# Kernel optimization log

Hardware: AMD Instinct MI355X
Metric: run time of the kernel (lower is better)

Reference implementation:

```python
import jax, jax.numpy as jnp
import numpy as np
import math

# config constants (match init_kwargs)
N_HEAD = 16
KNN_NUM = 4
MEM_FRAC = 4.0
BOOKKEEPING_FRAC = 0.0
RESID_ONLY = False
RESID_FOUND = 0.5   # set_resid_frac(resid_frac): found/current mix
RESID_CURR = 0.5
KNN_INFLUENCE = 1.0
NEG_INF = jnp.finfo(jnp.float32).min


def setup_inputs() -> dict:
    key = jax.random.key(0)
    k1, k2, k3, k4, k5 = jax.random.split(key, 5)
    B, T, C = 1, 2048, 1024
    H, d = N_HEAD, C // N_HEAD
    M = 8192  # per-head memory-store entries
    return {
        "x": jax.random.normal(k1, (B, T, C), jnp.float32),
        "c_attn_w": jax.random.normal(k2, (3 * C, C), jnp.float32) * 0.02,
        "c_proj_w": jax.random.normal(k3, (C, C), jnp.float32) * 0.02,
        "key_store": jax.random.normal(k4, (H, M, d), jnp.float32),
        "value_store": jax.random.normal(k5, (H, M, d), jnp.float32),
    }


def _knn_get(att, k, q, v, key_store, value_store):
    # att: (B,H,T,T), k/q/v: (B,H,T,d), stores: (H,M,d). B must be 1 (original
    # scatter offset i*t is only consistent for b==1).
    B, H, T, d = k.shape
    scale = 1.0 / math.sqrt(d)
    att_last = att[:, :, -1, :]                     # (B,H,T) last-query column
    # bookkeeping_frac == 0.0 -> skipped; mem_frac truthy -> threshold filter
    mask = att_last >= (1.0 / (MEM_FRAC * T))       # nonzero after zeroing

    # per-head flattened token lists, shape (H, N=B*T, d)
    kh = jnp.swapaxes(k, 0, 1).reshape(H, B * T, d)
    qh = jnp.swapaxes(q, 0, 1).reshape(H, B * T, d)
    vh = jnp.swapaxes(v, 0, 1).reshape(H, B * T, d)
    mask_h = jnp.swapaxes(mask, 0, 1).reshape(H, B * T)

    # exact L2 kNN (FAISS IndexFlatL2 equivalent): d2[h,n,m] = ||kh - ks||^2
    d2 = (jnp.sum(kh * kh, -1)[:, :, None]
          - 2.0 * jnp.einsum('hnd,hmd->hnm', kh, key_store)
          + jnp.sum(key_store * key_store, -1)[:, None, :])
    _, idx = jax.lax.top_k(-d2, KNN_NUM)            # (H,N,K) nearest indices

    h_ix = jnp.arange(H)[:, None, None]
    keys_found = key_store[h_ix, idx]               # (H,N,K,d)
    vals_found = value_store[h_ix, idx]
    keys_found = jnp.moveaxis(keys_found, 2, 0)     # (K,H,N,d)
    vals_found = jnp.moveaxis(vals_found, 2, 0)
    if not RESID_ONLY:
        keys_found = jnp.concatenate([kh[None], keys_found], axis=0)  # (K+1,H,N,d)
        vals_found = jnp.concatenate([vh[None], vals_found], axis=0)

    attf = jnp.einsum('khnd,hnd->khn', keys_found, qh) * scale
    attf = jnp.where(jnp.isnan(attf), NEG_INF, attf)
    attf = jax.nn.softmax(attf * KNN_INFLUENCE, axis=0)
    vals_new = jnp.einsum('khn,khnd->hnd', attf, vals_found)
    if RESID_FOUND > 0 or RESID_CURR > 0:
        vals_new = vals_new * RESID_FOUND + vh * RESID_CURR

    v_out = jnp.where(mask_h[..., None], vals_new, vh)   # scatter-equivalent
    return jnp.swapaxes(v_out.reshape(H, B, T, d), 0, 1)  # (B,H,T,d)


def reference(x, c_attn_w, c_proj_w, key_store, value_store):
    B, T, C = x.shape
    H, d = N_HEAD, C // N_HEAD
    qkv = x @ c_attn_w.T                             # (B,T,3C)
    q, k, v = jnp.split(qkv, 3, axis=2)
    q = jnp.swapaxes(q.reshape(B, T, H, d), 1, 2)    # (B,H,T,d)
    k = jnp.swapaxes(k.reshape(B, T, H, d), 1, 2)
    v = jnp.swapaxes(v.reshape(B, T, H, d), 1, 2)

    att = jnp.einsum('bhqd,bhkd->bhqk', q, k) * (1.0 / math.sqrt(d))
    causal = jnp.tril(jnp.ones((T, T), bool))
    att = jnp.where(causal, att, NEG_INF)
    att = jax.nn.softmax(att, axis=-1)

    # knn_get is @torch.no_grad() in the original -> stop_gradient
    v_new = jax.lax.stop_gradient(
        _knn_get(att, k, q, v, key_store, value_store))

    y = jnp.einsum('bhqk,bhkd->bhqd', att, v_new)
    y = jnp.swapaxes(y, 1, 2).reshape(B, T, C)
    return y @ c_proj_w.T
```

## Files before the change

kernel.cpp:

```cpp
#include <hip/hip_runtime.h>
#include <hip/hip_bf16.h>
#include <math.h>

#define TT 2048
#define CC 1024
#define HH 16
#define DDIM 64
#define MM 8192
#define C3 3072
#define SBIAS 256.0f

typedef __bf16 bf16x8 __attribute__((ext_vector_type(8)));
typedef float f32x4 __attribute__((ext_vector_type(4)));

__device__ __forceinline__ float waveReduceSum(float v) {
#pragma unroll
  for (int off = 32; off > 0; off >>= 1) v += __shfl_xor(v, off, 64);
  return v;
}
__device__ __forceinline__ unsigned umn(unsigned a, unsigned b){ return a<b?a:b; }
__device__ __forceinline__ unsigned umx(unsigned a, unsigned b){ return a>b?a:b; }
__device__ __forceinline__ unsigned umed3(unsigned a, unsigned b, unsigned c){
  unsigned d;
  asm("v_med3_u32 %0, %1, %2, %3" : "=v"(d) : "v"(a), "v"(b), "v"(c));
  return d;
}

__device__ __forceinline__ void gload16(const void* g, void* l) {
  __builtin_amdgcn_global_load_lds(
      (const __attribute__((address_space(1))) unsigned int*)g,
      (__attribute__((address_space(3))) unsigned int*)l, 16, 0, 0);
}

__global__ __launch_bounds__(256) void conv_split_k(const float* __restrict__ src,
    __hip_bfloat16* __restrict__ hi, __hip_bfloat16* __restrict__ lo)
{
  size_t i = (size_t)blockIdx.x*256 + threadIdx.x;
  const float4* p = (const float4*)(src + i*8);
  float4 a = p[0], b = p[1];
  float v[8] = {a.x,a.y,a.z,a.w,b.x,b.y,b.z,b.w};
  bf16x8 H, L;
#pragma unroll
  for (int e = 0; e < 8; ++e) {
    __bf16 hb = (__bf16)v[e];
    H[e] = hb;
    L[e] = (__bf16)(v[e] - (float)hb);
  }
  *reinterpret_cast<bf16x8*>(hi + i*8) = H;
  *reinterpret_cast<bf16x8*>(lo + i*8) = L;
}

__global__ __launch_bounds__(256) void conv_bf16_k(const float* __restrict__ src,
    __hip_bfloat16* __restrict__ dst)
{
  size_t i = (size_t)blockIdx.x*256 + threadIdx.x;
  const float4* p = (const float4*)(src + i*8);
  float4 a = p[0], b = p[1];
  float v[8] = {a.x,a.y,a.z,a.w,b.x,b.y,b.z,b.w};
  bf16x8 H;
#pragma unroll
  for (int e = 0; e < 8; ++e) H[e] = (__bf16)v[e];
  *reinterpret_cast<bf16x8*>(dst + i*8) = H;
}

__global__ __launch_bounds__(256) void conv_ks_k(const float* __restrict__ ks,
    __hip_bfloat16* __restrict__ ksb, float* __restrict__ ksn, unsigned* __restrict__ knhl)
{
  int row = blockIdx.x*4 + (threadIdx.x>>6);
  int lane = threadIdx.x & 63;
  float v = ks[(size_t)row*64 + lane];
  float sq = waveReduceSum(v*v);
  ksb[(size_t)row*64 + lane] = __float2bfloat16(-2.f*v);
  if (lane == 0) {
    ksn[row] = sq;
    float b = sq + SBIAS;
    __hip_bfloat16 hb = __float2bfloat16(b);
    float hf = __bfloat162float(hb);
    __hip_bfloat16 lb = __float2bfloat16(b - hf);
    unsigned h16 = (unsigned)__builtin_bit_cast(unsigned short, hb);
    unsigned l16 = (unsigned)__builtin_bit_cast(unsigned short, lb);
    knhl[row] = (l16 << 16) | h16;
  }
}

__global__ __launch_bounds__(256) void conv_kb_k(const float* __restrict__ qkv,
    __hip_bfloat16* __restrict__ kb)
{
  int e = blockIdx.x*256 + threadIdx.x;
  int dg = e & 7; int t = (e>>3) & (TT-1); int h = e >> 14;
  const float* src = qkv + (size_t)t*C3 + CC + h*64 + dg*8;
  __hip_bfloat16* dst = kb + ((size_t)(h*TT + t)*64 + dg*8);
#pragma unroll
  for (int i = 0; i < 8; ++i) dst[i] = __float2bfloat16(src[i]);
}

__global__ __launch_bounds__(256) void vtrans_k(const float* __restrict__ vnew,
    __hip_bfloat16* __restrict__ vbT)
{
  __shared__ float tbuf[64][65];
  const int h = blockIdx.y, t0 = blockIdx.x*64, tid = threadIdx.x;
#pragma unroll
  for (int r = 0; r < 16; ++r) {
    int e = r*256 + tid; int row = e>>6, dv = e&63;
    tbuf[row][dv] = vnew[((size_t)h*TT + t0 + row)*64 + dv];
  }
  __syncthreads();
#pragma unroll
  for (int r = 0; r < 16; ++r) {
    int e = r*256 + tid; int dv = e>>6, tt = e&63;
    vbT[((size_t)h*64 + dv)*TT + t0 + tt] = __float2bfloat16(tbuf[tt][dv]);
  }
}

template<bool SPLIT>
__global__ __launch_bounds__(256) void gemm_mfma_k(
    const __hip_bfloat16* __restrict__ Ah, const __hip_bfloat16* __restrict__ Al,
    const __hip_bfloat16* __restrict__ Bh, const __hip_bfloat16* __restrict__ Bl,
    float* __restrict__ Cc, int M, int N, int K)
{
  __shared__ __align__(16) char lds[2][32768];
  const int tid = threadIdx.x;
  const int nbx = N >> 7;
  const int by = blockIdx.x / nbx, bx = blockIdx.x - by*nbx;
  const int m0 = by << 7, n0 = bx << 7;
  const int w = tid >> 6;
  const int l = tid & 63;
  const int wslot = w << 6;
  const int wi = w >> 1, wj = w & 1;
  const int fr = l & 15, fo = l >> 4;
  const int kw = SPLIT ? 32 : 64;
  const int nsteps = K / kw;

  f32x4 acc[4][4];
#pragma unroll
  for (int i = 0; i < 4; ++i)
#pragma unroll
    for (int j = 0; j < 4; ++j) acc[i][j] = f32x4{0.f,0.f,0.f,0.f};

  int srow[4], schg[4];
#pragma unroll
  for (int r = 0; r < 4; ++r) {
    int s = r*256 + tid;
    srow[r] = s >> 3;
    schg[r] = (s & 7) ^ (srow[r] & 7);
  }

  auto stageAB = [&](int buf, int st) {
    const int k0 = st * kw;
#pragma unroll
    for (int r = 0; r < 4; ++r) {
      const __hip_bfloat16 *pa, *pb;
      if (SPLIT) {
        pa = (schg[r] < 4 ? Ah : Al) + (size_t)(m0+srow[r])*K + k0 + (schg[r]&3)*8;
        pb = (schg[r] < 4 ? Bh : Bl) + (size_t)(n0+srow[r])*K + k0 + (schg[r]&3)*8;
      } else {
        pa = Ah + (size_t)(m0+srow[r])*K + k0 + schg[r]*8;
        pb = Bh + (size_t)(n0+srow[r])*K + k0 + schg[r]*8;
      }
      gload16(pa, lds[buf] + (r*256 + wslot)*16);
      gload16(pb, lds[buf] + 16384 + (r*256 + wslot)*16);
    }
  };

  stageAB(0, 0);
  __syncthreads();

  for (int st = 0; st < nsteps; ++st) {
    const int buf = st & 1;
    if (st + 1 < nsteps) stageAB(buf ^ 1, st + 1);
    char* ldsb = lds[buf];

    if (SPLIT) {
      bf16x8 bhf[4], blf[4];
#pragma unroll
      for (int j = 0; j < 4; ++j) {
        int row = wj*64 + j*16 + fr;
        bhf[j] = *(const bf16x8*)(ldsb + 16384 + row*128 + ((fo     ^ (row&7))*16));
        blf[j] = *(const bf16x8*)(ldsb + 16384 + row*128 + (((4+fo) ^ (row&7))*16));
      }
#pragma unroll
      for (int i = 0; i < 4; ++i) {
        int row = wi*64 + i*16 + fr;
        bf16x8 ah = *(const bf16x8*)(ldsb + row*128 + ((fo     ^ (row&7))*16));
        bf16x8 al = *(const bf16x8*)(ldsb + row*128 + (((4+fo) ^ (row&7))*16));
#pragma unroll
        for (int j = 0; j < 4; ++j) {
          acc[i][j] = __builtin_amdgcn_mfma_f32_16x16x32_bf16(al, bhf[j], acc[i][j], 0,0,0);
          acc[i][j] = __builtin_amdgcn_mfma_f32_16x16x32_bf16(ah, blf[j], acc[i][j], 0,0,0);
          acc[i][j] = __builtin_amdgcn_mfma_f32_16x16x32_bf16(ah, bhf[j], acc[i][j], 0,0,0);
        }
      }
    } else {
#pragma unroll
      for (int kk = 0; kk < 2; ++kk) {
        bf16x8 bf[4];
#pragma unroll
        for (int j = 0; j < 4; ++j) {
          int row = wj*64 + j*16 + fr;
          bf[j] = *(const bf16x8*)(ldsb + 16384 + row*128 + (((kk*4+fo) ^ (row&7))*16));
        }
#pragma unroll
        for (int i = 0; i < 4; ++i) {
          int row = wi*64 + i*16 + fr;
          bf16x8 af = *(const bf16x8*)(ldsb + row*128 + (((kk*4+fo) ^ (row&7))*16));
#pragma unroll
          for (int j = 0; j < 4; ++j)
            acc[i][j] = __builtin_amdgcn_mfma_f32_16x16x32_bf16(af, bf[j], acc[i][j], 0,0,0);
        }
      }
    }
    __syncthreads();
  }

  float* ep = (float*)((char*)lds + (size_t)w*8704);
#pragma unroll
  for (int pass = 0; pass < 2; ++pass) {
#pragma unroll
    for (int ii = 0; ii < 2; ++ii) {
      int i = pass*2 + ii;
#pragma unroll
      for (int j = 0; j < 4; ++j)
#pragma unroll
        for (int e = 0; e < 4; ++e)
          ep[(ii*16 + fo*4 + e)*68 + j*16 + fr] = acc[i][j][e];
    }
#pragma unroll
    for (int eidx = 0; eidx < 8; ++eidx) {
      int fi = eidx*64 + l;
      int row = fi >> 4, c4 = fi & 15;
      float4 v4 = *(const float4*)(ep + row*68 + c4*4);
      *(float4*)(Cc + (size_t)(m0 + wi*64 + pass*32 + row)*N + n0 + wj*64 + c4*4) = v4;
    }
  }
}

__global__ __launch_bounds__(256) void attlast_mask_k(const float* __restrict__ qkv, int* __restrict__ mask)
{
  const int h = blockIdx.x;
  __shared__ float ql[64];
  __shared__ float lg[TT];
  __shared__ float red[256];
  const int tid = threadIdx.x;
  if (tid < 64) ql[tid] = qkv[(size_t)(TT-1)*C3 + h*DDIM + tid];
  __syncthreads();
  float lmax = -INFINITY;
  for (int t = tid; t < TT; t += 256) {
    const float* kr = qkv + (size_t)t*C3 + CC + h*DDIM;
    float s = 0.f;
#pragma unroll
    for (int d = 0; d < 64; ++d) s += ql[d] * kr[d];
    s *= 0.125f;
    lg[t] = s;
    lmax = fmaxf(lmax, s);
  }
  red[tid] = lmax; __syncthreads();
  for (int off = 128; off > 0; off >>= 1) { if (tid < off) red[tid] = fmaxf(red[tid], red[tid+off]); __syncthreads(); }
  float mx = red[0];
  __syncthreads();
  float ls = 0.f;
  for (int t = tid; t < TT; t += 256) { float e = expf(lg[t]-mx); lg[t] = e; ls += e; }
  red[tid] = ls; __syncthreads();
  for (int off = 128; off > 0; off >>= 1) { if (tid < off) red[tid] += red[tid+off]; __syncthreads(); }
  float Z = red[0];
  for (int t = tid; t < TT; t += 256) mask[h*TT + t] = (lg[t]/Z >= 1.220703125e-4f) ? 1 : 0;
}

__global__ __launch_bounds__(256) void knn_chunkmin_k(
    const __hip_bfloat16* __restrict__ kb, const __hip_bfloat16* __restrict__ ksb,
    const unsigned* __restrict__ knhl, unsigned int* __restrict__ cand)
{
  __shared__ __align__(16) char lds[2*8192];
  const int tid = threadIdx.x;
  const int bid = blockIdx.x;
  const int orig = (bid & 7)*64 + (bid >> 3);
  const int h  = orig >> 5;
  const int n0 = (orig & 31) * 64;
  const int w  = tid >> 6;
  const int l  = tid & 63;
  const int cr = l & 15, hi = l >> 4;

  bf16x8 af0, af1;
  {
    const __hip_bfloat16* kbh = kb + (size_t)h*TT*64 + (size_t)(n0 + w*16 + cr)*64;
    af0 = *reinterpret_cast<const bf16x8*>(kbh + hi*8);
    af1 = *reinterpret_cast<const bf16x8*>(kbh + 32 + hi*8);
  }
  bf16x8 aext;
  {
    uint4 t = { (l < 16) ? 0x3F803F80u : 0u, 0u, 0u, 0u };
    aext = __builtin_bit_cast(bf16x8, t);
  }
  const __hip_bfloat16* ksbh = ksb + (size_t)h*MM*64;
  const unsigned* knh = knhl + (size_t)h*MM;

  const int s0 = tid, s1 = tid + 256;
  const int g0 = (s0 & ~7) | ((s0 & 7) ^ ((s0 >> 3) & 7));
  const int g1 = (s1 & ~7) | ((s1 & 7) ^ ((s1 >> 3) & 7));
  const int rb0 = (l&15)*128 + ((hi ^ (l&7))*16);
  const int rb1 = (l&15)*128 + (((4+hi) ^ (l&7))*16);

  unsigned cnd[4][4];
#pragma unroll
  for (int i = 0; i < 4; ++i)
#pragma unroll
    for (int c = 0; c < 4; ++c) cnd[i][c] = 0xFFFFFFFFu;

  auto stage = [&](int buf, int tt) {
    const __hip_bfloat16* src = ksbh + (size_t)tt*4096;
    gload16(src + g0*8, lds + buf*8192 + (w << 10));
    gload16(src + g1*8, lds + buf*8192 + 4096 + (w << 10));
  };

  stage(0, 0);
  __syncthreads();

  for (int tt = 0; tt < 128; ++tt) {
    const int buf = tt & 1;
    if (tt + 1 < 128) stage(buf ^ 1, tt + 1);
    char* ldsb = lds + buf*8192;
    const unsigned crtt = ((unsigned)cr << 7) | (unsigned)tt;

    f32x4 acc[4];
#pragma unroll
    for (int b = 0; b < 4; ++b) {
      uint4 kt = { knh[tt*64 + b*16 + cr], 0u, 0u, 0u };
      bf16x8 bext = __builtin_bit_cast(bf16x8, kt);
      bf16x8 bf0 = *reinterpret_cast<const bf16x8*>(ldsb + b*2048 + rb0);
      bf16x8 bf1 = *reinterpret_cast<const bf16x8*>(ldsb + b*2048 + rb1);
      f32x4 z = {0.f, 0.f, 0.f, 0.f};
      z = __builtin_amdgcn_mfma_f32_16x16x32_bf16(aext, bext, z, 0, 0, 0);
      z = __builtin_amdgcn_mfma_f32_16x16x32_bf16(af0, bf0, z, 0, 0, 0);
      z = __builtin_amdgcn_mfma_f32_16x16x32_bf16(af1, bf1, z, 0, 0, 0);
      acc[b] = z;
    }
#pragma unroll
    for (int i = 0; i < 4; ++i) {
      float m4 = fminf(fminf(fminf(acc[0][i], acc[1][i]), acc[2][i]), acc[3][i]);
      unsigned x = (__float_as_uint(m4) & 0xFFFFF800u) | crtt;
      unsigned t0 = umn(cnd[i][0], x);
      unsigned t1 = umed3(x, cnd[i][0], cnd[i][1]);
      unsigned t2 = umed3(x, cnd[i][1], cnd[i][2]);
      unsigned t3 = umed3(x, cnd[i][2], cnd[i][3]);
      cnd[i][0] = t0; cnd[i][1] = t1; cnd[i][2] = t2; cnd[i][3] = t3;
    }
    __syncthreads();
  }

#pragma unroll
  for (int i = 0; i < 4; ++i) {
    int n = n0 + w*16 + hi*4 + i;
    reinterpret_cast<uint4*>(cand)[(size_t)(h*TT + n)*16 + cr] =
        make_uint4(cnd[i][0], cnd[i][1], cnd[i][2], cnd[i][3]);
  }
}

__global__ __launch_bounds__(256) void knn_fused_k(
    const unsigned int* __restrict__ cand, const float* __restrict__ qkv,
    const float* __restrict__ kstore, const float* __restrict__ vstore,
    const float* __restrict__ ksn, const int* __restrict__ mask,
    float* __restrict__ vnew)
{
  const int row = blockIdx.x*4 + (threadIdx.x>>6);
  const int l = threadIdx.x & 63;
  const int h = row >> 11, t = row & (TT-1);
  const float* base = qkv + (size_t)t*C3 + h*64;
  float vh = base[2*CC + l];
  float* outp = vnew + (size_t)row*64;
  if (!mask[row]) { outp[l] = vh; return; }

  unsigned v = cand[(size_t)row*64 + l];
#pragma unroll
  for (int k = 2; k <= 64; k <<= 1)
#pragma unroll
    for (int j = k>>1; j > 0; j >>= 1) {
      unsigned o = __shfl_xor(v, j, 64);
      bool takeMin = ((l & j) == 0) == ((l & k) == 0);
      v = (takeMin == (o < v)) ? o : v;
    }

  const int c = l >> 1;
  const int b = c & 3;
  unsigned vc = __shfl(v, c >> 2, 64);
  const int m = ((int)(vc & 127u))*64 + b*16 + (int)((vc >> 7) & 15u);
  const int p = l & 1;
  {
    const float* kq = base + CC + p*32;
    const float* ksr = kstore + ((size_t)h*MM + m)*64 + p*32;
    float dp = 0.f;
#pragma unroll
    for (int i = 0; i < 8; ++i) {
      float4 a = *(const float4*)(kq + i*4);
      float4 bb = *(const float4*)(ksr + i*4);
      dp = fmaf(a.x,bb.x, fmaf(a.y,bb.y, fmaf(a.z,bb.z, fmaf(a.w,bb.w, dp))));
    }
    dp += __shfl_xor(dp, 1, 64);
    float s = ksn[(size_t)h*MM + m] - 2.f*dp;
    unsigned u = __float_as_uint(s);
    unsigned skey = u ^ (unsigned)(((int)u >> 31) | 0x80000000);
    unsigned khi = (p == 0) ? skey : 0xFFFFFFFFu;
    unsigned klo = (p == 0) ? (unsigned)m : 0xFFFFFFFFu;
#pragma unroll
    for (int k = 2; k <= 64; k <<= 1)
#pragma unroll
      for (int j = k>>1; j > 0; j >>= 1) {
        unsigned oh = __shfl_xor(khi, j, 64);
        unsigned ol = __shfl_xor(klo, j, 64);
        bool takeMin = ((l & j) == 0) == ((l & k) == 0);
        bool oLess = (oh < khi) || (oh == khi && ol < klo);
        if (takeMin == oLess) { khi = oh; klo = ol; }
      }
    v = klo;
  }

  const int m0 = (int)__shfl(v, 0, 64);
  const int m1 = (int)__shfl(v, 1, 64);
  const int m2 = (int)__shfl(v, 2, 64);
  const int m3 = (int)__shfl(v, 3, 64);
  const int g = l >> 3, gl = l & 7;
  float dq = 0.f;
  if (g < 5) {
    int msel = (g == 0) ? m0 : (g == 1) ? m1 : (g == 2) ? m2 : m3;
    const float* qrow = base + gl*8;
    const float* kr = (g < 4) ? (kstore + ((size_t)h*MM + msel)*64 + gl*8)
                              : (base + CC + gl*8);
    float4 a0 = *(const float4*)(qrow);
    float4 a1 = *(const float4*)(qrow + 4);
    float4 b0 = *(const float4*)(kr);
    float4 b1 = *(const float4*)(kr + 4);
    dq = a0.x*b0.x + a0.y*b0.y + a0.z*b0.z + a0.w*b0.w
       + a1.x*b1.x + a1.y*b1.y + a1.z*b1.z + a1.w*b1.w;
  }
  dq += __shfl_xor(dq, 1, 64);
  dq += __shfl_xor(dq, 2, 64);
  dq += __shfl_xor(dq, 4, 64);
  float d0 = __shfl(dq,  0, 64)*0.125f;
  float d1 = __shfl(dq,  8, 64)*0.125f;
  float d2 = __shfl(dq, 16, 64)*0.125f;
  float d3 = __shfl(dq, 24, 64)*0.125f;
  float d4 = __shfl(dq, 32, 64)*0.125f;
  float mx = fmaxf(fmaxf(fmaxf(d0,d1),fmaxf(d2,d3)),d4);
  float w0 = expf(d0-mx), w1 = expf(d1-mx), w2 = expf(d2-mx),
        w3 = expf(d3-mx), w4 = expf(d4-mx);
  float Z = w0+w1+w2+w3+w4;
  float vv = w4*vh
           + w0*vstore[((size_t)h*MM+m0)*64 + l]
           + w1*vstore[((size_t)h*MM+m1)*64 + l]
           + w2*vstore[((size_t)h*MM+m2)*64 + l]
           + w3*vstore[((size_t)h*MM+m3)*64 + l];
  outp[l] = 0.5f*(vv/Z) + 0.5f*vh;
}

__global__ __launch_bounds__(256) void attn_mfma_k(
    const float* __restrict__ qkv, const __hip_bfloat16* __restrict__ kb,
    const __hip_bfloat16* __restrict__ vbT, __hip_bfloat16* __restrict__ yb)
{
  __shared__ __align__(16) char lds[40960];
  const int h = blockIdx.y, bx = blockIdx.x, tid = threadIdx.x;
  const int w = tid>>6, l = tid&63, fr = l&15, fo = l>>4;
  const int wslot = w << 6;
  const __hip_bfloat16* kbh = kb + (size_t)h*TT*64;
  const __hip_bfloat16* vbh = vbT + (size_t)h*64*TT;
  char* Pt = lds + 32768 + w*2048;

  int srow[2], schg[2];
#pragma unroll
  for (int r = 0; r < 2; ++r) {
    int s = r*256 + tid;
    srow[r] = s >> 3;
    schg[r] = (s & 7) ^ (srow[r] & 7);
  }

  auto stageKV = [&](int buf, int kt) {
#pragma unroll
    for (int r = 0; r < 2; ++r) {
      gload16(kbh + (size_t)(kt*64 + srow[r])*64 + schg[r]*8,
              lds + buf*16384 + (r*256 + wslot)*16);
      gload16(vbh + (size_t)srow[r]*TT + kt*64 + schg[r]*8,
              lds + buf*16384 + 8192 + (r*256 + wslot)*16);
    }
  };

  for (int half = 0; half < 2; ++half) {
    const int qblk = half ? (31 - bx) : bx;
    const int q0 = qblk * 64;
    bf16x8 qa[2];
    {
      const float* qrow = qkv + (size_t)(q0 + w*16 + fr)*C3 + h*64;
#pragma unroll
      for (int kk = 0; kk < 2; ++kk) {
        float4 u0 = *(const float4*)(qrow + kk*32 + fo*8);
        float4 u1 = *(const float4*)(qrow + kk*32 + fo*8 + 4);
        bf16x8 t;
        t[0]=(__bf16)u0.x; t[1]=(__bf16)u0.y; t[2]=(__bf16)u0.z; t[3]=(__bf16)u0.w;
        t[4]=(__bf16)u1.x; t[5]=(__bf16)u1.y; t[6]=(__bf16)u1.z; t[7]=(__bf16)u1.w;
        qa[kk] = t;
      }
    }
    float mrow[4], lsum[4];
    f32x4 oacc[4];
#pragma unroll
    for (int e = 0; e < 4; ++e) { mrow[e] = -INFINITY; lsum[e] = 0.f; }
#pragma unroll
    for (int jv = 0; jv < 4; ++jv) oacc[jv] = f32x4{0.f,0.f,0.f,0.f};

    const int ntiles = qblk + 1;
    stageKV(0, 0);
    __syncthreads();

    for (int kt = 0; kt < ntiles; ++kt) {
      const int buf = kt & 1;
      if (kt + 1 < ntiles) stageKV(buf ^ 1, kt + 1);
      char* Kt = lds + buf*16384;
      char* Vt = Kt + 8192;

      f32x4 sv[4];
#pragma unroll
      for (int j = 0; j < 4; ++j) {
        int row = j*16 + fr;
        bf16x8 k0f = *(const bf16x8*)(Kt + row*128 + ((fo     ^ (row&7))*16));
        bf16x8 k1f = *(const bf16x8*)(Kt + row*128 + (((4+fo) ^ (row&7))*16));
        f32x4 z = {0.f,0.f,0.f,0.f};
        z = __builtin_amdgcn_mfma_f32_16x16x32_bf16(qa[0], k0f, z, 0,0,0);
        z = __builtin_amdgcn_mfma_f32_16x16x32_bf16(qa[1], k1f, z, 0,0,0);
        sv[j] = z;
      }
      if (kt == qblk) {
#pragma unroll
        for (int j = 0; j < 4; ++j)
#pragma unroll
          for (int e = 0; e < 4; ++e)
            sv[j][e] = (j*16 + fr <= w*16 + fo*4 + e) ? sv[j][e]*0.125f : -INFINITY;
      } else {
#pragma unroll
        for (int j = 0; j < 4; ++j)
#pragma unroll
          for (int e = 0; e < 4; ++e) sv[j][e] *= 0.125f;
      }
      float rmax[4];
#pragma unroll
      for (int e = 0; e < 4; ++e)
        rmax[e] = fmaxf(fmaxf(sv[0][e], sv[1][e]), fmaxf(sv[2][e], sv[3][e]));
#pragma unroll
      for (int off = 1; off < 16; off <<= 1)
#pragma unroll
        for (int e = 0; e < 4; ++e) rmax[e] = fmaxf(rmax[e], __shfl_xor(rmax[e], off, 64));
      float scl[4];
#pragma unroll
      for (int e = 0; e < 4; ++e) {
        float mn = fmaxf(mrow[e], rmax[e]);
        scl[e] = __expf(mrow[e] - mn);
        mrow[e] = mn;
      }
      float rsum[4] = {0.f,0.f,0.f,0.f};
#pragma unroll
      for (int j = 0; j < 4; ++j) {
        int chunkbase = j*2 + (fr>>3);
        int kvoff = (fr&7)*2;
#pragma unroll
        for (int e = 0; e < 4; ++e) {
          float p = __expf(sv[j][e] - mrow[e]);
          rsum[e] += p;
          int qloc = fo*4 + e;
          *(__bf16*)(Pt + qloc*128 + ((chunkbase ^ (qloc&7))*16) + kvoff) = (__bf16)p;
        }
      }
#pragma unroll
      for (int off = 1; off < 16; off <<= 1)
#pragma unroll
        for (int e = 0; e < 4; ++e) rsum[e] += __shfl_xor(rsum[e], off, 64);
#pragma unroll
      for (int e = 0; e < 4; ++e) lsum[e] = lsum[e]*scl[e] + rsum[e];
#pragma unroll
      for (int jv = 0; jv < 4; ++jv)
#pragma unroll
        for (int e = 0; e < 4; ++e) oacc[jv][e] *= scl[e];

      bf16x8 pa0 = *(const bf16x8*)(Pt + fr*128 + ((fo     ^ (fr&7))*16));
      bf16x8 pa1 = *(const bf16x8*)(Pt + fr*128 + (((4+fo) ^ (fr&7))*16));
#pragma unroll
      for (int jv = 0; jv < 4; ++jv) {
        int row = jv*16 + fr;
        bf16x8 v0f = *(const bf16x8*)(Vt + row*128 + ((fo     ^ (row&7))*16));
        bf16x8 v1f = *(const bf16x8*)(Vt + row*128 + (((4+fo) ^ (row&7))*16));
        oacc[jv] = __builtin_amdgcn_mfma_f32_16x16x32_bf16(pa0, v0f, oacc[jv], 0,0,0);
        oacc[jv] = __builtin_amdgcn_mfma_f32_16x16x32_bf16(pa1, v1f, oacc[jv], 0,0,0);
      }
      __syncthreads();
    }
#pragma unroll
    for (int jv = 0; jv < 4; ++jv)
#pragma unroll
      for (int e = 0; e < 4; ++e) {
        int t = q0 + w*16 + fo*4 + e;
        yb[(size_t)t*CC + h*64 + jv*16 + fr] = __float2bfloat16(oacc[jv][e] / lsum[e]);
      }
  }
}

extern "C" void kernel_launch(void* const* d_in, const int* in_sizes, int n_in,
                              void* d_out, int out_size, void* d_ws, size_t ws_size,
                              hipStream_t stream) {
  const float* x   = (const float*)d_in[0];
  const float* wat = (const float*)d_in[1];
  const float* wpr = (const float*)d_in[2];
  const float* kst = (const float*)d_in[3];
  const float* vst = (const float*)d_in[4];
  float* out = (float*)d_out;

  float* ws    = (float*)d_ws;
  float* qkv   = ws;
  float* ksn   = qkv + (size_t)6291456;
  unsigned* knhl = (unsigned*)(ksn + 131072);
  int*   idxb  = (int*)(knhl + 131072);
  int*   maskb = idxb + 131072;
  __hip_bfloat16* kb = (__hip_bfloat16*)(maskb + 32768);
  float* candRegion = (float*)kb + 1048576;
  unsigned int* candb = (unsigned int*)candRegion;
  float* vnew = candRegion;
  __hip_bfloat16* vbT = (__hip_bfloat16*)(candRegion + 2097152);
  float* split = candRegion + 2097152 + 1048576;
  __hip_bfloat16* xhi = (__hip_bfloat16*)split;
  __hip_bfloat16* xlo = xhi + 2097152;
  __hip_bfloat16* whi = xlo + 2097152;
  __hip_bfloat16* wlo = whi + 3145728;
  __hip_bfloat16* ksb  = (__hip_bfloat16*)split;
  __hip_bfloat16* wprb = ksb + 8388608;
  __hip_bfloat16* yb   = (__hip_bfloat16*)split;

  conv_split_k<<<dim3(1024), 256, 0, stream>>>(x, xhi, xlo);
  conv_split_k<<<dim3(1536), 256, 0, stream>>>(wat, whi, wlo);
  gemm_mfma_k<true><<<dim3(16*24), 256, 0, stream>>>(xhi, xlo, whi, wlo, qkv, TT, C3, CC);
  conv_kb_k<<<dim3(1024), 256, 0, stream>>>(qkv, kb);
  conv_ks_k<<<dim3(HH*MM/4), 256, 0, stream>>>(kst, ksb, ksn, knhl);
  conv_bf16_k<<<dim3(512), 256, 0, stream>>>(wpr, wprb);
  attlast_mask_k<<<dim3(HH), 256, 0, stream>>>(qkv, maskb);
  knn_chunkmin_k<<<dim3(512), 256, 0, stream>>>(kb, ksb, knhl, candb);
  knn_fused_k<<<dim3(HH*TT/4), 256, 0, stream>>>(candb, qkv, kst, vst, ksn, maskb, vnew);
  vtrans_k<<<dim3(32, HH), 256, 0, stream>>>(vnew, vbT);
  attn_mfma_k<<<dim3(16, HH), 256, 0, stream>>>(qkv, kb, vbT, yb);
  gemm_mfma_k<false><<<dim3(16*8), 256, 0, stream>>>(yb, nullptr, wprb, nullptr, out, TT, CC, CC);
}
```

Before: 357.0 us.

## Split kNN key-store scan across wave pairs and add norms in fp32

The kNN chunk-min kernel now gives each block 32 query rows instead of 64 and splits the 8192-entry key store between two wave pairs. Grid size doubles, raising occupancy and parallelism. The two partial top-4 lists are combined through LDS with a reversed elementwise min, which yields the correct four smallest but unsorted. The extra MFMA that folded the bias plus squared norm in as a bf16 hi/lo pair is replaced by an fp32 fma with a per-entry norm loaded from global memory. Store keys are now kept unscaled in bf16, trading one matrix op per tile for a few VALU ops and scalar-ish loads.

```diff
diff --git a/kernel.cpp b/kernel.cpp
--- a/kernel.cpp
+++ b/kernel.cpp
@@ -19,7 +19,6 @@
   return v;
 }
 __device__ __forceinline__ unsigned umn(unsigned a, unsigned b){ return a<b?a:b; }
-__device__ __forceinline__ unsigned umx(unsigned a, unsigned b){ return a>b?a:b; }
 __device__ __forceinline__ unsigned umed3(unsigned a, unsigned b, unsigned c){
   unsigned d;
   asm("v_med3_u32 %0, %1, %2, %3" : "=v"(d) : "v"(a), "v"(b), "v"(c));
@@ -64,23 +63,14 @@
 }
 
 __global__ __launch_bounds__(256) void conv_ks_k(const float* __restrict__ ks,
-    __hip_bfloat16* __restrict__ ksb, float* __restrict__ ksn, unsigned* __restrict__ knhl)
+    __hip_bfloat16* __restrict__ ksb, float* __restrict__ ksn, float* __restrict__ ksnb)
 {
   int row = blockIdx.x*4 + (threadIdx.x>>6);
   int lane = threadIdx.x & 63;
   float v = ks[(size_t)row*64 + lane];
   float sq = waveReduceSum(v*v);
-  ksb[(size_t)row*64 + lane] = __float2bfloat16(-2.f*v);
-  if (lane == 0) {
-    ksn[row] = sq;
-    float b = sq + SBIAS;
-    __hip_bfloat16 hb = __float2bfloat16(b);
-    float hf = __bfloat162float(hb);
-    __hip_bfloat16 lb = __float2bfloat16(b - hf);
-    unsigned h16 = (unsigned)__builtin_bit_cast(unsigned short, hb);
-    unsigned l16 = (unsigned)__builtin_bit_cast(unsigned short, lb);
-    knhl[row] = (l16 << 16) | h16;
-  }
+  ksb[(size_t)row*64 + lane] = __float2bfloat16(v);
+  if (lane == 0) { ksn[row] = sq; ksnb[row] = sq + SBIAS; }
 }
 
 __global__ __launch_bounds__(256) void conv_kb_k(const float* __restrict__ qkv,
@@ -267,37 +257,38 @@
 
 __global__ __launch_bounds__(256) void knn_chunkmin_k(
     const __hip_bfloat16* __restrict__ kb, const __hip_bfloat16* __restrict__ ksb,
-    const unsigned* __restrict__ knhl, unsigned int* __restrict__ cand)
-{
-  __shared__ __align__(16) char lds[2*8192];
+    const float* __restrict__ ksnb, unsigned int* __restrict__ cand)
+{
+  __shared__ __align__(16) char lds[32768];
   const int tid = threadIdx.x;
   const int bid = blockIdx.x;
-  const int orig = (bid & 7)*64 + (bid >> 3);
-  const int h  = orig >> 5;
-  const int n0 = (orig & 31) * 64;
+  const int orig = (bid & 7)*128 + (bid >> 3);
+  const int h  = orig >> 6;
+  const int n0 = (orig & 63) * 32;
   const int w  = tid >> 6;
+  const int wh = w >> 1;
+  const int wr = w & 1;
   const int l  = tid & 63;
   const int cr = l & 15, hi = l >> 4;
 
   bf16x8 af0, af1;
   {
-    const __hip_bfloat16* kbh = kb + (size_t)h*TT*64 + (size_t)(n0 + w*16 + cr)*64;
+    const __hip_bfloat16* kbh = kb + (size_t)h*TT*64 + (size_t)(n0 + wr*16 + cr)*64;
     af0 = *reinterpret_cast<const bf16x8*>(kbh + hi*8);
     af1 = *reinterpret_cast<const bf16x8*>(kbh + 32 + hi*8);
   }
-  bf16x8 aext;
-  {
-    uint4 t = { (l < 16) ? 0x3F803F80u : 0u, 0u, 0u, 0u };
-    aext = __builtin_bit_cast(bf16x8, t);
-  }
   const __hip_bfloat16* ksbh = ksb + (size_t)h*MM*64;
-  const unsigned* knh = knhl + (size_t)h*MM;
-
-  const int s0 = tid, s1 = tid + 256;
-  const int g0 = (s0 & ~7) | ((s0 & 7) ^ ((s0 >> 3) & 7));
-  const int g1 = (s1 & ~7) | ((s1 & 7) ^ ((s1 >> 3) & 7));
-  const int rb0 = (l&15)*128 + ((hi ^ (l&7))*16);
-  const int rb1 = (l&15)*128 + (((4+hi) ^ (l&7))*16);
+  const float* ksnh = ksnb + (size_t)h*MM;
+
+  char* myhalf = lds + wh*16384;
+  int gsrc[4];
+#pragma unroll
+  for (int r = 0; r < 4; ++r) {
+    int s = r*128 + wr*64 + l;
+    gsrc[r] = (s & ~7) | ((s & 7) ^ ((s >> 3) & 7));
+  }
+  const int rb0 = cr*128 + ((hi ^ (l&7))*16);
+  const int rb1 = cr*128 + (((4+hi) ^ (l&7))*16);
 
   unsigned cnd[4][4];
 #pragma unroll
@@ -306,36 +297,45 @@
     for (int c = 0; c < 4; ++c) cnd[i][c] = 0xFFFFFFFFu;
 
   auto stage = [&](int buf, int tt) {
-    const __hip_bfloat16* src = ksbh + (size_t)tt*4096;
-    gload16(src + g0*8, lds + buf*8192 + (w << 10));
-    gload16(src + g1*8, lds + buf*8192 + 4096 + (w << 10));
+    const __hip_bfloat16* src = ksbh + ((size_t)(wh*64 + tt))*4096;
+    char* dst = myhalf + buf*8192 + (wr << 10);
+#pragma unroll
+    for (int r = 0; r < 4; ++r)
+      gload16(src + gsrc[r]*8, dst + (r << 11));
   };
 
   stage(0, 0);
   __syncthreads();
 
-  for (int tt = 0; tt < 128; ++tt) {
+  for (int tt = 0; tt < 64; ++tt) {
     const int buf = tt & 1;
-    if (tt + 1 < 128) stage(buf ^ 1, tt + 1);
-    char* ldsb = lds + buf*8192;
-    const unsigned crtt = ((unsigned)cr << 7) | (unsigned)tt;
+    if (tt + 1 < 64) stage(buf ^ 1, tt + 1);
+    char* ldsb = myhalf + buf*8192;
+    const int ttg = wh*64 + tt;
+    const unsigned crtt = ((unsigned)cr << 7) | (unsigned)ttg;
+
+    float kn0 = ksnh[ttg*64 +  0 + cr];
+    float kn1 = ksnh[ttg*64 + 16 + cr];
+    float kn2 = ksnh[ttg*64 + 32 + cr];
+    float kn3 = ksnh[ttg*64 + 48 + cr];
 
     f32x4 acc[4];
 #pragma unroll
     for (int b = 0; b < 4; ++b) {
-      uint4 kt = { knh[tt*64 + b*16 + cr], 0u, 0u, 0u };
-      bf16x8 bext = __builtin_bit_cast(bf16x8, kt);
       bf16x8 bf0 = *reinterpret_cast<const bf16x8*>(ldsb + b*2048 + rb0);
       bf16x8 bf1 = *reinterpret_cast<const bf16x8*>(ldsb + b*2048 + rb1);
       f32x4 z = {0.f, 0.f, 0.f, 0.f};
-      z = __builtin_amdgcn_mfma_f32_16x16x32_bf16(aext, bext, z, 0, 0, 0);
       z = __builtin_amdgcn_mfma_f32_16x16x32_bf16(af0, bf0, z, 0, 0, 0);
       z = __builtin_amdgcn_mfma_f32_16x16x32_bf16(af1, bf1, z, 0, 0, 0);
       acc[b] = z;
     }
 #pragma unroll
     for (int i = 0; i < 4; ++i) {
-      float m4 = fminf(fminf(fminf(acc[0][i], acc[1][i]), acc[2][i]), acc[3][i]);
+      float s0 = fmaf(acc[0][i], -2.f, kn0);
+      float s1 = fmaf(acc[1][i], -2.f, kn1);
+      float s2 = fmaf(acc[2][i], -2.f, kn2);
+      float s3 = fmaf(acc[3][i], -2.f, kn3);
+      float m4 = fminf(fminf(s0, s1), fminf(s2, s3));
       unsigned x = (__float_as_uint(m4) & 0xFFFFF800u) | crtt;
       unsigned t0 = umn(cnd[i][0], x);
       unsigned t1 = umed3(x, cnd[i][0], cnd[i][1]);
@@ -346,11 +346,22 @@
     __syncthreads();
   }
 
-#pragma unroll
-  for (int i = 0; i < 4; ++i) {
-    int n = n0 + w*16 + hi*4 + i;
-    reinterpret_cast<uint4*>(cand)[(size_t)(h*TT + n)*16 + cr] =
-        make_uint4(cnd[i][0], cnd[i][1], cnd[i][2], cnd[i][3]);
+  uint4* sh = (uint4*)lds;
+  if (wh == 1) {
+#pragma unroll
+    for (int i = 0; i < 4; ++i)
+      sh[wr*256 + (hi*4+i)*16 + cr] = make_uint4(cnd[i][0], cnd[i][1], cnd[i][2], cnd[i][3]);
+  }
+  __syncthreads();
+  if (wh == 0) {
+#pragma unroll
+    for (int i = 0; i < 4; ++i) {
+      uint4 b = sh[wr*256 + (hi*4+i)*16 + cr];
+      int n = n0 + wr*16 + hi*4 + i;
+      reinterpret_cast<uint4*>(cand)[(size_t)(h*TT + n)*16 + cr] =
+          make_uint4(umn(cnd[i][0], b.w), umn(cnd[i][1], b.z),
+                     umn(cnd[i][2], b.y), umn(cnd[i][3], b.x));
+    }
   }
 }
 
@@ -610,8 +621,8 @@
   float* ws    = (float*)d_ws;
   float* qkv   = ws;
   float* ksn   = qkv + (size_t)6291456;
-  unsigned* knhl = (unsigned*)(ksn + 131072);
-  int*   idxb  = (int*)(knhl + 131072);
+  float* ksnb  = ksn + 131072;
+  int*   idxb  = (int*)(ksnb + 131072);
   int*   maskb = idxb + 131072;
   __hip_bfloat16* kb = (__hip_bfloat16*)(maskb + 32768);
   float* candRegion = (float*)kb + 1048576;
@@ -631,10 +642,10 @@
   conv_split_k<<<dim3(1536), 256, 0, stream>>>(wat, whi, wlo);
   gemm_mfma_k<true><<<dim3(16*24), 256, 0, stream>>>(xhi, xlo, whi, wlo, qkv, TT, C3, CC);
   conv_kb_k<<<dim3(1024), 256, 0, stream>>>(qkv, kb);
-  conv_ks_k<<<dim3(HH*MM/4), 256, 0, stream>>>(kst, ksb, ksn, knhl);
+  conv_ks_k<<<dim3(HH*MM/4), 256, 0, stream>>>(kst, ksb, ksn, ksnb);
   conv_bf16_k<<<dim3(512), 256, 0, stream>>>(wpr, wprb);
   attlast_mask_k<<<dim3(HH), 256, 0, stream>>>(qkv, maskb);
-  knn_chunkmin_k<<<dim3(512), 256, 0, stream>>>(kb, ksb, knhl, candb);
+  knn_chunkmin_k<<<dim3(1024), 256, 0, stream>>>(kb, ksb, ksnb, candb);
   knn_fused_k<<<dim3(HH*TT/4), 256, 0, stream>>>(candb, qkv, kst, vst, ksn, maskb, vnew);
   vtrans_k<<<dim3(32, HH), 256, 0, stream>>>(vnew, vbT);
   attn_mfma_k<<<dim3(16, HH), 256, 0, stream>>>(qkv, kb, vbT, yb);
```

Result: faster. 305.7 us (-14.4%).
